# Performance work log

Hardware: AMD Instinct MI355X
Metric: run time of the kernel (lower is better)

## Reference

```python
import jax, jax.numpy as jnp
import numpy as np

N_NODES = 100000
N_EDGES = 1600000
IN_FEATS = 256
N_HIDDEN = 128
N_CLASSES = 40


def setup_inputs() -> dict:
    key = jax.random.key(0)
    k1, k2, k3, k4, k5 = jax.random.split(key, 5)
    features = jax.random.normal(k1, (N_NODES, IN_FEATS), dtype=jnp.float32)
    edge_src = jax.random.randint(k2, (N_EDGES,), 0, N_NODES, dtype=jnp.int64)
    edge_dst = jax.random.randint(k3, (N_EDGES,), 0, N_NODES, dtype=jnp.int64)
    # GraphConv weights (Glorot-ish scaling)
    W1 = jax.random.normal(k4, (IN_FEATS, N_HIDDEN), dtype=jnp.float32) / np.sqrt(IN_FEATS)
    b1 = jnp.zeros((N_HIDDEN,), dtype=jnp.float32)
    W2 = jax.random.normal(k5, (N_HIDDEN, N_CLASSES), dtype=jnp.float32) / np.sqrt(N_HIDDEN)
    b2 = jnpspace = None
    b2 = jnp.zeros((N_CLASSES,), dtype=jnp.float32)
    return {"features": features, "edge_src": edge_src, "edge_dst": edge_dst,
            "W1": W1, "b1": b1, "W2": W2, "b2": b2}


def _degree_norms(edge_src, edge_dst, n_nodes):
    ones = jnp.ones(edge_src.shape[0], dtype=jnp.float32)
    deg_out = jax.ops.segment_sum(ones, edge_src, num_segments=n_nodes)
    deg_in = jax.ops.segment_sum(ones, edge_dst, num_segments=n_nodes)
    norm_src = jax.lax.rsqrt(jnp.clip(deg_out, 1.0))  # D_out^{-1/2}
    norm_dst = jax.lax.rsqrt(jnp.clip(deg_in, 1.0))   # D_in^{-1/2}
    return norm_src, norm_dst


def _graph_conv(x, W, b, edge_src, edge_dst, norm_src, norm_dst, activation=None):
    # DGL GraphConv norm='both': out = D_in^{-1/2} A D_out^{-1/2} (x W) + b
    h = (x @ W) * norm_src[:, None]                       # transform then src-normalize
    agg = jax.ops.segment_sum(h[edge_src], edge_dst,
                              num_segments=x.shape[0])    # sparse neighbor aggregation
    out = agg * norm_dst[:, None] + b
    if activation is not None:
        out = activation(out)
    return out


def reference(features, edge_src, edge_dst, W1, b1, W2, b2):
    norm_src, norm_dst = _degree_norms(edge_src, edge_dst, features.shape[0])
    h = _graph_conv(features, W1, b1, edge_src, edge_dst, norm_src, norm_dst,
                    activation=jax.nn.relu)
    # dropout is identity in eval-mode reference
    out = _graph_conv(h, W2, b2, edge_src, edge_dst, norm_src, norm_dst)
    return out
```

## Files before the change

### kernel.cpp

```cpp
#include <hip/hip_runtime.h>
#include <hip/hip_bf16.h>
#include <hip/hip_fp16.h>

#define NN 100000
#define NE 1600000
#define KF 256
#define NH 128
#define NC 40
#define PAD 64
#define CMAX 63

#define NBLK_P 512
#define PCHUNK (NE / NBLK_P)
#define BUK 256
#define NBUK ((NN + BUK - 1) / BUK)
#define CAP 6144

typedef __attribute__((ext_vector_type(8))) short bf16x8;
typedef __attribute__((ext_vector_type(4))) float f32x4;


__device__ __forceinline__ float ldf(const void* p, size_t i, bool bf){
  return bf ? __bfloat162float(((const __hip_bfloat16*)p)[i]) : ((const float*)p)[i];
}
__device__ __forceinline__ void cv2(unsigned int v, float* o){
  union { unsigned int i; float f; } a, b;
  a.i = v << 16; b.i = v & 0xffff0000u;
  o[0] = a.f; o[1] = b.f;
}

__global__ void k_sniff_edges(const unsigned int* __restrict__ e, unsigned int* __restrict__ flags){
  __shared__ unsigned int sh[256];
  unsigned int v = 0;
  for (int i = blockIdx.x * 256 + threadIdx.x; i < NE / 2; i += gridDim.x * 256)
    v |= e[2 * i + 1];
  sh[threadIdx.x] = v;
  __syncthreads();
  for (int off = 128; off; off >>= 1){
    if (threadIdx.x < off) sh[threadIdx.x] |= sh[threadIdx.x + off];
    __syncthreads();
  }
  if (threadIdx.x == 0 && sh[0]) atomicOr(&flags[0], sh[0]);
}

__global__ void k_sniff_float(const unsigned int* __restrict__ w, unsigned int* __restrict__ flags){
  __shared__ unsigned int sh[256];
  unsigned int hits = 0;
  for (int i = blockIdx.x * 256 + threadIdx.x; i < (1 << 20); i += gridDim.x * 256){
    unsigned int b = (w[i] >> 7) & 0xFFu;
    hits += (b >= 118u && b <= 130u) ? 1u : 0u;
  }
  sh[threadIdx.x] = hits;
  __syncthreads();
  for (int off = 128; off; off >>= 1){
    if (threadIdx.x < off) sh[threadIdx.x] += sh[threadIdx.x + off];
    __syncthreads();
  }
  if (threadIdx.x == 0) atomicAdd(&flags[1], sh[0]);
}

__device__ __forceinline__ int edge_at(const void* p, int e, bool is64){
  return is64 ? (int)((const long long*)p)[e] : ((const int*)p)[e];
}
__device__ __forceinline__ bool f_isbf(const unsigned int* flags){ return flags[1] > (1u << 19); }

__global__ __launch_bounds__(256) void k_part(const void* __restrict__ src,
    const void* __restrict__ dst, const unsigned int* __restrict__ flags,
    int* __restrict__ deg_out, int* __restrict__ gcur, unsigned int* __restrict__ part){
  __shared__ int cnt[NBUK];
  __shared__ int base[NBUK];
  const bool is64 = (flags[0] == 0u);
  const int beg = blockIdx.x * PCHUNK;
  const int end = min(beg + PCHUNK, NE);
  for (int t = threadIdx.x; t < NBUK; t += 256) cnt[t] = 0;
  __syncthreads();
  for (int e = beg + threadIdx.x; e < end; e += 256){
    int d = edge_at(dst, e, is64);
    atomicAdd(&cnt[d >> 8], 1);
  }
  __syncthreads();
  for (int t = threadIdx.x; t < NBUK; t += 256){
    int c = cnt[t];
    base[t] = c ? atomicAdd(&gcur[t], c) : 0;
    cnt[t] = 0;
  }
  __syncthreads();
  for (int e = beg + threadIdx.x; e < end; e += 256){
    int d = edge_at(dst, e, is64);
    int s = edge_at(src, e, is64);
    atomicAdd(&deg_out[s], 1);
    int b = d >> 8;
    int pos = base[b] + atomicAdd(&cnt[b], 1);
    if (pos < CAP)
      part[(size_t)b * CAP + pos] = ((unsigned int)s << 8) | (unsigned int)(d & 255);
  }
}

__global__ __launch_bounds__(256) void k_csr(const unsigned int* __restrict__ part,
    const int* __restrict__ gcur, int* __restrict__ fill, int* __restrict__ csr_pad){
  __shared__ int rows[256 * CMAX];
  __shared__ int fl[256];
  const int b = blockIdx.x;
  fl[threadIdx.x] = 0;
  __syncthreads();
  const int n = min(gcur[b], CAP);
  for (int i = threadIdx.x; i < n; i += 256){
    unsigned int e = part[(size_t)b * CAP + i];
    int r = (int)(e & 255u);
    int s = (int)(e >> 8);
    int pos = atomicAdd(&fl[r], 1);
    if (pos < CMAX) rows[r * CMAX + pos] = s;
  }
  __syncthreads();
  const int node0 = b * BUK;
  if (node0 + threadIdx.x < NN) fill[node0 + threadIdx.x] = fl[threadIdx.x];
  for (int idx = threadIdx.x; idx < 256 * CMAX; idx += 256){
    int r = idx / CMAX;
    int c = idx - r * CMAX;
    int node = node0 + r;
    if (node < NN) csr_pad[node * PAD + c] = rows[idx];
  }
}

__global__ void k_norms(const int* __restrict__ deg_out, const int* __restrict__ fill,
                        float* __restrict__ nsrc, float* __restrict__ ndst){
  int i = blockIdx.x * 256 + threadIdx.x;
  if (i < NN){
    nsrc[i] = rsqrtf(fmaxf((float)deg_out[i], 1.f));
    ndst[i] = rsqrtf(fmaxf((float)fill[i], 1.f));
  }
}

__global__ void k_w1s(const void* __restrict__ W1, const unsigned int* __restrict__ flags,
                      bf16x8* __restrict__ w1s){
  if (!f_isbf(flags)) return;
  int idx = blockIdx.x * 256 + threadIdx.x;
  if (idx >= 4096) return;
  int l    = idx & 63;
  int tile = idx >> 6;
  int kt   = tile >> 3;
  int nt   = tile & 7;
  int krow = kt * 32 + (l >> 4) * 8;
  int col  = nt * 16 + (l & 15);
  const unsigned short* w = (const unsigned short*)W1;
  bf16x8 v;
  #pragma unroll
  for (int j = 0; j < 8; j++)
    v[j] = (short)w[(size_t)(krow + j) * NH + col];
  w1s[idx] = v;
}

__global__ __launch_bounds__(256) void k_gemm1_mfma(const void* __restrict__ feat,
    const bf16x8* __restrict__ w1s, const unsigned int* __restrict__ flags,
    const float* __restrict__ nsrc, __half* __restrict__ h1){
  if (!f_isbf(flags)) return;
  const int t  = threadIdx.x;
  const int wv = t >> 6;
  const int l  = t & 63;
  const int row0 = blockIdx.x * 64 + wv * 16;
  const int arow = row0 + (l & 15);
  const short* fp = (const short*)feat;
  const size_t abase = (size_t)min(arow, NN - 1) * KF + (l >> 4) * 8;

  f32x4 acc[8];
  #pragma unroll
  for (int n = 0; n < 8; n++) acc[n] = (f32x4){0.f, 0.f, 0.f, 0.f};

  #pragma unroll 2
  for (int kt = 0; kt < 8; kt++){
    bf16x8 a = *(const bf16x8*)(fp + abase + kt * 32);
    #pragma unroll
    for (int n = 0; n < 8; n++){
      bf16x8 b = w1s[(kt * 8 + n) * 64 + l];
      acc[n] = __builtin_amdgcn_mfma_f32_16x16x32_bf16(a, b, acc[n], 0, 0, 0);
    }
  }
  const int rbase = row0 + (l >> 4) * 4;
  const int col   = l & 15;
  #pragma unroll
  for (int i = 0; i < 4; i++){
    int r = rbase + i;
    if (r < NN){
      float s = nsrc[r];
      #pragma unroll
      for (int n = 0; n < 8; n++)
        h1[(size_t)r * NH + n * 16 + col] = __float2half_rn(acc[n][i] * s);
    }
  }
}

__global__ __launch_bounds__(256) void k_gemm1(const void* __restrict__ feat,
    const void* __restrict__ W1, const unsigned int* __restrict__ flags,
    const float* __restrict__ nsrc, __half* __restrict__ h1){
  if (f_isbf(flags)) return;
  __shared__ float As[64][68];
  __shared__ float Bs[64][128];
  const int t = threadIdx.x;
  const int row0 = blockIdx.x * 64;
  const int cg = t & 15;
  const int rg = t >> 4;
  float acc[4][8];
  #pragma unroll
  for (int i = 0; i < 4; i++)
    #pragma unroll
    for (int j = 0; j < 8; j++) acc[i][j] = 0.f;

  const int ar   = t >> 2;
  const int ak   = (t & 3) * 16;
  const int arow = row0 + ar;

  for (int kc = 0; kc < KF; kc += 64){
    if (arow < NN){
      size_t off = (size_t)arow * KF + kc + ak;
      const float4* p = (const float4*)((const float*)feat + off);
      float4 v0 = p[0], v1 = p[1], v2 = p[2], v3 = p[3];
      *(float4*)&As[ar][ak +  0] = v0;
      *(float4*)&As[ar][ak +  4] = v1;
      *(float4*)&As[ar][ak +  8] = v2;
      *(float4*)&As[ar][ak + 12] = v3;
    } else {
      #pragma unroll
      for (int j = 0; j < 16; j++) As[ar][ak + j] = 0.f;
    }
    #pragma unroll
    for (int q0 = 0; q0 < 8; q0++){
      int q  = t + q0 * 256;
      int bk = q >> 5;
      int bc = (q & 31) * 4;
      *(float4*)&Bs[bk][bc] = *(const float4*)((const float*)W1 + (size_t)(kc + bk) * NH + bc);
    }
    __syncthreads();
    #pragma unroll 8
    for (int k = 0; k < 64; k++){
      float a0 = As[rg*4+0][k];
      float a1 = As[rg*4+1][k];
      float a2 = As[rg*4+2][k];
      float a3 = As[rg*4+3][k];
      float b[8];
      #pragma unroll
      for (int j = 0; j < 8; j++) b[j] = Bs[k][cg*8 + j];
      #pragma unroll
      for (int j = 0; j < 8; j++){
        acc[0][j] += a0 * b[j];
        acc[1][j] += a1 * b[j];
        acc[2][j] += a2 * b[j];
        acc[3][j] += a3 * b[j];
      }
    }
    __syncthreads();
  }
  #pragma unroll
  for (int i = 0; i < 4; i++){
    int r = row0 + rg*4 + i;
    if (r < NN){
      float s = nsrc[r];
      __half2* op = (__half2*)(h1 + (size_t)r * NH) + cg*4;
      #pragma unroll
      for (int j = 0; j < 4; j++)
        op[j] = __floats2half2_rn(acc[i][2*j] * s, acc[i][2*j+1] * s);
    }
  }
}

__global__ __launch_bounds__(256) void k_agg1(const int* __restrict__ csr_pad,
    const int* __restrict__ fill, const float* __restrict__ ndst,
    const unsigned int* __restrict__ h1w, const void* __restrict__ b1,
    const unsigned int* __restrict__ flags, float* __restrict__ x1){
  const bool isbf = f_isbf(flags);
  int node = blockIdx.x * 4 + (threadIdx.x >> 6);
  if (node >= NN) return;
  int lane = threadIdx.x & 63;
  int beg = node * PAD;
  int end = beg + min(fill[node], CMAX);
  float ax0 = 0.f, ay0 = 0.f, ax1 = 0.f, ay1 = 0.f;
  int e = beg;
  for (; e + 2 <= end; e += 2){
    int s0 = csr_pad[e], s1 = csr_pad[e+1];
    unsigned int u0 = h1w[(size_t)s0 * (NH/2) + lane];
    unsigned int u1 = h1w[(size_t)s1 * (NH/2) + lane];
    float2 v0 = __half22float2(*(__half2*)&u0);
    float2 v1 = __half22float2(*(__half2*)&u1);
    ax0 += v0.x; ay0 += v0.y;
    ax1 += v1.x; ay1 += v1.y;
  }
  if (e < end){
    int s0 = csr_pad[e];
    unsigned int u0 = h1w[(size_t)s0 * (NH/2) + lane];
    float2 v0 = __half22float2(*(__half2*)&u0);
    ax0 += v0.x; ay0 += v0.y;
  }
  float nd = ndst[node];
  float bx = ldf(b1, lane*2,   isbf);
  float by = ldf(b1, lane*2+1, isbf);
  float2 o;
  o.x = fmaxf((ax0 + ax1) * nd + bx, 0.f);
  o.y = fmaxf((ay0 + ay1) * nd + by, 0.f);
  ((float2*)(x1 + (size_t)node * NH))[lane] = o;
}

__global__ __launch_bounds__(256) void k_gemm2(const float* __restrict__ x1,
    const void* __restrict__ W2, const unsigned int* __restrict__ flags,
    const float* __restrict__ nsrc, __half* __restrict__ h2){
  const bool isbf = f_isbf(flags);
  __shared__ float Xs[128][68];
  __shared__ float Ws[64][44];
  const int t = threadIdx.x;
  const int row0 = blockIdx.x * 128;
  const int cg = t & 7;
  const int rg = t >> 3;
  float acc[4][5];
  #pragma unroll
  for (int i = 0; i < 4; i++)
    #pragma unroll
    for (int j = 0; j < 5; j++) acc[i][j] = 0.f;

  for (int kc = 0; kc < NH; kc += 64){
    #pragma unroll
    for (int q0 = 0; q0 < 8; q0++){
      int q  = t + q0 * 256;
      int r  = q >> 4;
      int kq = (q & 15) * 4;
      int grow = row0 + r;
      float4 v;
      if (grow < NN) v = *(const float4*)(x1 + (size_t)grow * NH + kc + kq);
      else { v.x = v.y = v.z = v.w = 0.f; }
      *(float4*)&Xs[r][kq] = v;
    }
    #pragma unroll
    for (int q0 = 0; q0 < 10; q0++){
      int idx = t + q0 * 256;
      int k = idx / 40;
      int c = idx - k * 40;
      Ws[k][c] = ldf(W2, (size_t)(kc + k) * NC + c, isbf);
    }
    __syncthreads();
    #pragma unroll 4
    for (int k = 0; k < 64; k++){
      float a0 = Xs[rg*4+0][k];
      float a1 = Xs[rg*4+1][k];
      float a2 = Xs[rg*4+2][k];
      float a3 = Xs[rg*4+3][k];
      float b[5];
      #pragma unroll
      for (int j = 0; j < 5; j++) b[j] = Ws[k][cg*5 + j];
      #pragma unroll
      for (int j = 0; j < 5; j++){
        acc[0][j] += a0 * b[j];
        acc[1][j] += a1 * b[j];
        acc[2][j] += a2 * b[j];
        acc[3][j] += a3 * b[j];
      }
    }
    __syncthreads();
  }
  #pragma unroll
  for (int i = 0; i < 4; i++){
    int r = row0 + rg*4 + i;
    if (r < NN){
      float s = nsrc[r];
      #pragma unroll
      for (int j = 0; j < 5; j++)
        h2[(size_t)r * NC + cg*5 + j] = __float2half_rn(acc[i][j] * s);
    }
  }
}

__global__ __launch_bounds__(256) void k_agg2(const int* __restrict__ csr_pad,
    const int* __restrict__ fill, const float* __restrict__ ndst,
    const unsigned int* __restrict__ h2w, const void* __restrict__ b2,
    const unsigned int* __restrict__ flags, float* __restrict__ out){
  const bool isbf = f_isbf(flags);
  int node = blockIdx.x * 4 + (threadIdx.x >> 6);
  if (node >= NN) return;
  int lane = threadIdx.x & 63;
  int beg = node * PAD;
  int end = beg + min(fill[node], CMAX);
  if (lane < NC/2){
    float ax0 = 0.f, ay0 = 0.f, ax1 = 0.f, ay1 = 0.f;
    int e = beg;
    for (; e + 2 <= end; e += 2){
      int s0 = csr_pad[e], s1 = csr_pad[e+1];
      unsigned int u0 = h2w[(size_t)s0 * (NC/2) + lane];
      unsigned int u1 = h2w[(size_t)s1 * (NC/2) + lane];
      float2 v0 = __half22float2(*(__half2*)&u0);
      float2 v1 = __half22float2(*(__half2*)&u1);
      ax0 += v0.x; ay0 += v0.y;
      ax1 += v1.x; ay1 += v1.y;
    }
    if (e < end){
      int s0 = csr_pad[e];
      unsigned int u0 = h2w[(size_t)s0 * (NC/2) + lane];
      float2 v0 = __half22float2(*(__half2*)&u0);
      ax0 += v0.x; ay0 += v0.y;
    }
    float nd = ndst[node];
    float2 o;
    o.x = (ax0 + ax1) * nd + ldf(b2, 2*lane,   isbf);
    o.y = (ay0 + ay1) * nd + ldf(b2, 2*lane+1, isbf);
    ((float2*)(out + (size_t)node * NC))[lane] = o;
  }
}

extern "C" void kernel_launch(void* const* d_in, const int* in_sizes, int n_in,
                              void* d_out, int out_size, void* d_ws, size_t ws_size,
                              hipStream_t stream) {
  const long long SZ_FEAT = (long long)NN * KF, SZ_E = NE, SZ_W1 = (long long)KF * NH,
                  SZ_B1 = NH, SZ_W2 = (long long)NH * NC, SZ_B2 = NC;
  int i_feat = -1, i_e1 = -1, i_e2 = -1, i_W1 = -1, i_b1 = -1, i_W2 = -1, i_b2 = -1;
  auto m = [](long long s, long long z){ return s == z || s == 4*z || s == 8*z || s == 2*z; };
  for (int i = 0; i < n_in; i++){
    long long s = in_sizes[i];
    if      (m(s, SZ_FEAT)) i_feat = i;
    else if (m(s, SZ_E))    { if (i_e1 < 0) i_e1 = i; else i_e2 = i; }
    else if (m(s, SZ_W1))   i_W1 = i;
    else if (m(s, SZ_B1))   i_b1 = i;
    else if (m(s, SZ_W2))   i_W2 = i;
    else if (m(s, SZ_B2))   i_b2 = i;
  }
  if (i_feat < 0 || i_e2 < 0 || i_W1 < 0 || i_b1 < 0 || i_W2 < 0 || i_b2 < 0){
    i_feat = 0; i_e1 = 1; i_e2 = 2; i_W1 = 3; i_b1 = 4; i_W2 = 5; i_b2 = 6;
  }
  const void* feat = d_in[i_feat];
  const void* esrc = d_in[i_e1];
  const void* edst = d_in[i_e2];
  const void* W1   = d_in[i_W1];
  const void* b1   = d_in[i_b1];
  const void* W2   = d_in[i_W2];
  const void* b2   = d_in[i_b2];
  float* out = (float*)d_out;

  int* deg_out        = (int*)d_ws;
  int* fill           = deg_out + NN;
  unsigned int* flags = (unsigned int*)(fill + NN);
  int* gcur           = (int*)(flags + 4);
  float* norm_src     = (float*)(gcur + 400);
  float* norm_dst     = norm_src + NN;
  int* csr_pad        = (int*)(norm_dst + NN);
  __half* h1          = (__half*)(csr_pad + (size_t)NN * PAD);
  float* x1           = (float*)(h1 + (size_t)NN * NH);
  __half* h2          = h1;
  unsigned int* part  = (unsigned int*)x1;
  bf16x8* w1s         = (bf16x8*)((char*)x1 + (16u << 20));

  hipMemsetAsync(deg_out, 0, ((size_t)2 * NN + 4 + 400) * sizeof(int), stream);

  k_sniff_edges<<<400, 256, 0, stream>>>((const unsigned int*)esrc, flags);
  k_sniff_float<<<256, 256, 0, stream>>>((const unsigned int*)feat, flags);
  k_w1s <<<16, 256, 0, stream>>>(W1, flags, w1s);
  k_part<<<NBLK_P, 256, 0, stream>>>(esrc, edst, flags, deg_out, gcur, part);
  k_csr <<<NBUK,   256, 0, stream>>>(part, gcur, fill, csr_pad);
  k_norms<<<(NN + 255) / 256, 256, 0, stream>>>(deg_out, fill, norm_src, norm_dst);

  k_gemm1     <<<(NN + 63) / 64, 256, 0, stream>>>(feat, W1, flags, norm_src, h1);
  k_gemm1_mfma<<<(NN + 63) / 64, 256, 0, stream>>>(feat, w1s, flags, norm_src, h1);
  k_agg1 <<<(NN + 3) / 4, 256, 0, stream>>>(csr_pad, fill, norm_dst,
                                            (const unsigned int*)h1, b1, flags, x1);
  k_gemm2<<<(NN + 127) / 128, 256, 0, stream>>>(x1, W2, flags, norm_src, h2);
  k_agg2 <<<(NN + 3) / 4, 256, 0, stream>>>(csr_pad, fill, norm_dst,
                                            (const unsigned int*)h2, b2, flags, out);
}
```

Baseline: 594.2 us.

## Run fp32 first-layer GEMM on bf16 MFMA with hi/lo split emulation

Replaces the fp32 path of the first GEMM, which used scalar FMAs with LDS tiling, with an MFMA kernel. Each fp32 operand is split into high and low bf16 parts and combined as hi*hi + lo*hi + hi*lo, roughly matching fp32 accuracy. A new pre-pass builds swizzled hi/lo copies of W1, and each wave now covers 32 rows instead of 16. Costs are three MFMAs per product, extra conversion ALU work, and slightly lower precision than true fp32.

```diff
diff --git a/kernel.cpp b/kernel.cpp
--- a/kernel.cpp
+++ b/kernel.cpp
@@ -27,6 +27,13 @@
   union { unsigned int i; float f; } a, b;
   a.i = v << 16; b.i = v & 0xffff0000u;
   o[0] = a.f; o[1] = b.f;
+}
+__device__ __forceinline__ void splitbf(float f, short* h, short* lo){
+  union { float f; unsigned int u; } a; a.f = f;
+  *h = (short)(a.u >> 16);
+  union { unsigned int u; float f; } c; c.u = a.u & 0xffff0000u;
+  union { float f; unsigned int u; } d; d.f = f - c.f;
+  *lo = (short)(d.u >> 16);
 }
 
 __global__ void k_sniff_edges(const unsigned int* __restrict__ e, unsigned int* __restrict__ flags){
@@ -149,6 +156,28 @@
     v[j] = (short)w[(size_t)(krow + j) * NH + col];
   w1s[idx] = v;
 }
+__global__ void k_w1s_f32(const void* __restrict__ W1, const unsigned int* __restrict__ flags,
+                          bf16x8* __restrict__ w1h, bf16x8* __restrict__ w1l){
+  if (f_isbf(flags)) return;
+  int idx = blockIdx.x * 256 + threadIdx.x;
+  if (idx >= 4096) return;
+  int l    = idx & 63;
+  int tile = idx >> 6;
+  int kt   = tile >> 3;
+  int nt   = tile & 7;
+  int krow = kt * 32 + (l >> 4) * 8;
+  int col  = nt * 16 + (l & 15);
+  const float* w = (const float*)W1;
+  bf16x8 vh, vl;
+  #pragma unroll
+  for (int j = 0; j < 8; j++){
+    short h, lo;
+    splitbf(w[(size_t)(krow + j) * NH + col], &h, &lo);
+    vh[j] = h; vl[j] = lo;
+  }
+  w1h[idx] = vh;
+  w1l[idx] = vl;
+}
 
 __global__ __launch_bounds__(256) void k_gemm1_mfma(const void* __restrict__ feat,
     const bf16x8* __restrict__ w1s, const unsigned int* __restrict__ flags,
@@ -189,75 +218,75 @@
   }
 }
 
-__global__ __launch_bounds__(256) void k_gemm1(const void* __restrict__ feat,
-    const void* __restrict__ W1, const unsigned int* __restrict__ flags,
+__global__ __launch_bounds__(256) void k_gemm1_mf32(const float* __restrict__ feat,
+    const bf16x8* __restrict__ w1h, const bf16x8* __restrict__ w1l,
+    const unsigned int* __restrict__ flags,
     const float* __restrict__ nsrc, __half* __restrict__ h1){
   if (f_isbf(flags)) return;
-  __shared__ float As[64][68];
-  __shared__ float Bs[64][128];
-  const int t = threadIdx.x;
-  const int row0 = blockIdx.x * 64;
-  const int cg = t & 15;
-  const int rg = t >> 4;
-  float acc[4][8];
-  #pragma unroll
-  for (int i = 0; i < 4; i++)
-    #pragma unroll
-    for (int j = 0; j < 8; j++) acc[i][j] = 0.f;
-
-  const int ar   = t >> 2;
-  const int ak   = (t & 3) * 16;
-  const int arow = row0 + ar;
-
-  for (int kc = 0; kc < KF; kc += 64){
-    if (arow < NN){
-      size_t off = (size_t)arow * KF + kc + ak;
-      const float4* p = (const float4*)((const float*)feat + off);
-      float4 v0 = p[0], v1 = p[1], v2 = p[2], v3 = p[3];
-      *(float4*)&As[ar][ak +  0] = v0;
-      *(float4*)&As[ar][ak +  4] = v1;
-      *(float4*)&As[ar][ak +  8] = v2;
-      *(float4*)&As[ar][ak + 12] = v3;
-    } else {
-      #pragma unroll
-      for (int j = 0; j < 16; j++) As[ar][ak + j] = 0.f;
-    }
-    #pragma unroll
-    for (int q0 = 0; q0 < 8; q0++){
-      int q  = t + q0 * 256;
-      int bk = q >> 5;
-      int bc = (q & 31) * 4;
-      *(float4*)&Bs[bk][bc] = *(const float4*)((const float*)W1 + (size_t)(kc + bk) * NH + bc);
-    }
-    __syncthreads();
-    #pragma unroll 8
-    for (int k = 0; k < 64; k++){
-      float a0 = As[rg*4+0][k];
-      float a1 = As[rg*4+1][k];
-      float a2 = As[rg*4+2][k];
-      float a3 = As[rg*4+3][k];
-      float b[8];
-      #pragma unroll
-      for (int j = 0; j < 8; j++) b[j] = Bs[k][cg*8 + j];
-      #pragma unroll
-      for (int j = 0; j < 8; j++){
-        acc[0][j] += a0 * b[j];
-        acc[1][j] += a1 * b[j];
-        acc[2][j] += a2 * b[j];
-        acc[3][j] += a3 * b[j];
+  const int t  = threadIdx.x;
+  const int wv = t >> 6;
+  const int l  = t & 63;
+  const int row0 = blockIdx.x * 128 + wv * 32;
+  const int ar0 = row0 + (l & 15);
+  const int ar1 = ar0 + 16;
+  const float* fp0 = feat + (size_t)min(ar0, NN - 1) * KF + (l >> 4) * 8;
+  const float* fp1 = feat + (size_t)min(ar1, NN - 1) * KF + (l >> 4) * 8;
+
+  f32x4 acc[2][8];
+  #pragma unroll
+  for (int g = 0; g < 2; g++)
+    #pragma unroll
+    for (int n = 0; n < 8; n++) acc[g][n] = (f32x4){0.f, 0.f, 0.f, 0.f};
+
+  for (int kt = 0; kt < 8; kt++){
+    float4 u0 = *(const float4*)(fp0 + kt * 32);
+    float4 u1 = *(const float4*)(fp0 + kt * 32 + 4);
+    float4 v0 = *(const float4*)(fp1 + kt * 32);
+    float4 v1 = *(const float4*)(fp1 + kt * 32 + 4);
+    bf16x8 a0h, a0l, a1h, a1l;
+    {
+      const float* uf = (const float*)&u0;
+      const float* vf = (const float*)&v0;
+      #pragma unroll
+      for (int j = 0; j < 4; j++){
+        short h, lo;
+        splitbf(uf[j], &h, &lo); a0h[j] = h; a0l[j] = lo;
+        splitbf(vf[j], &h, &lo); a1h[j] = h; a1l[j] = lo;
       }
-    }
-    __syncthreads();
-  }
-  #pragma unroll
-  for (int i = 0; i < 4; i++){
-    int r = row0 + rg*4 + i;
-    if (r < NN){
-      float s = nsrc[r];
-      __half2* op = (__half2*)(h1 + (size_t)r * NH) + cg*4;
-      #pragma unroll
-      for (int j = 0; j < 4; j++)
-        op[j] = __floats2half2_rn(acc[i][2*j] * s, acc[i][2*j+1] * s);
+      const float* uf2 = (const float*)&u1;
+      const float* vf2 = (const float*)&v1;
+      #pragma unroll
+      for (int j = 0; j < 4; j++){
+        short h, lo;
+        splitbf(uf2[j], &h, &lo); a0h[4 + j] = h; a0l[4 + j] = lo;
+        splitbf(vf2[j], &h, &lo); a1h[4 + j] = h; a1l[4 + j] = lo;
+      }
+    }
+    #pragma unroll
+    for (int n = 0; n < 8; n++){
+      bf16x8 bh = w1h[(kt * 8 + n) * 64 + l];
+      bf16x8 bl = w1l[(kt * 8 + n) * 64 + l];
+      acc[0][n] = __builtin_amdgcn_mfma_f32_16x16x32_bf16(a0h, bh, acc[0][n], 0, 0, 0);
+      acc[0][n] = __builtin_amdgcn_mfma_f32_16x16x32_bf16(a0l, bh, acc[0][n], 0, 0, 0);
+      acc[0][n] = __builtin_amdgcn_mfma_f32_16x16x32_bf16(a0h, bl, acc[0][n], 0, 0, 0);
+      acc[1][n] = __builtin_amdgcn_mfma_f32_16x16x32_bf16(a1h, bh, acc[1][n], 0, 0, 0);
+      acc[1][n] = __builtin_amdgcn_mfma_f32_16x16x32_bf16(a1l, bh, acc[1][n], 0, 0, 0);
+      acc[1][n] = __builtin_amdgcn_mfma_f32_16x16x32_bf16(a1h, bl, acc[1][n], 0, 0, 0);
+    }
+  }
+  const int col = l & 15;
+  #pragma unroll
+  for (int g = 0; g < 2; g++){
+    const int rbase = row0 + g * 16 + (l >> 4) * 4;
+    #pragma unroll
+    for (int i = 0; i < 4; i++){
+      int r = rbase + i;
+      if (r < NN){
+        float s = nsrc[r];
+        #pragma unroll
+        for (int n = 0; n < 8; n++)
+          h1[(size_t)r * NH + n * 16 + col] = __float2half_rn(acc[g][n][i] * s);
+      }
     }
   }
 }
@@ -440,19 +469,22 @@
   float* x1           = (float*)(h1 + (size_t)NN * NH);
   __half* h2          = h1;
   unsigned int* part  = (unsigned int*)x1;
-  bf16x8* w1s         = (bf16x8*)((char*)x1 + (16u << 20));
+  bf16x8* w1h         = (bf16x8*)((char*)x1 + (16u << 20));
+  bf16x8* w1l         = w1h + 4096;
 
   hipMemsetAsync(deg_out, 0, ((size_t)2 * NN + 4 + 400) * sizeof(int), stream);
 
   k_sniff_edges<<<400, 256, 0, stream>>>((const unsigned int*)esrc, flags);
   k_sniff_float<<<256, 256, 0, stream>>>((const unsigned int*)feat, flags);
-  k_w1s <<<16, 256, 0, stream>>>(W1, flags, w1s);
+  k_w1s    <<<16, 256, 0, stream>>>(W1, flags, w1h);
+  k_w1s_f32<<<16, 256, 0, stream>>>(W1, flags, w1h, w1l);
   k_part<<<NBLK_P, 256, 0, stream>>>(esrc, edst, flags, deg_out, gcur, part);
   k_csr <<<NBUK,   256, 0, stream>>>(part, gcur, fill, csr_pad);
   k_norms<<<(NN + 255) / 256, 256, 0, stream>>>(deg_out, fill, norm_src, norm_dst);
 
-  k_gemm1     <<<(NN + 63) / 64, 256, 0, stream>>>(feat, W1, flags, norm_src, h1);
-  k_gemm1_mfma<<<(NN + 63) / 64, 256, 0, stream>>>(feat, w1s, flags, norm_src, h1);
+  k_gemm1_mfma<<<(NN + 63) / 64,   256, 0, stream>>>(feat, w1h, flags, norm_src, h1);
+  k_gemm1_mf32<<<(NN + 127) / 128, 256, 0, stream>>>((const float*)feat, w1h, w1l,
+                                                     flags, norm_src, h1);
   k_agg1 <<<(NN + 3) / 4, 256, 0, stream>>>(csr_pad, fill, norm_dst,
                                             (const unsigned int*)h1, b1, flags, x1);
   k_gemm2<<<(NN + 127) / 128, 256, 0, stream>>>(x1, W2, flags, norm_src, h2);
```

Result: faster. 568.9 us (-4.3%).
